# Kernel optimization log

Hardware: AMD Instinct MI355X
Metric: run time of the kernel (lower is better)

The kernel has to match this reference:

```python
import jax, jax.numpy as jnp
import numpy as np

D_WIN = 4  # local_size (max displacement); (2*D_WIN+1)^2 = 81 displacements


def avg_pool4(x):
    B, C, H, W = x.shape
    return x.reshape(B, C, H // 4, 4, W // 4, 4).mean(axis=(3, 5))


def corr_max(cur, feats, d):
    """FlowNet-style correlation (kernel=1, pad=d, max_disp=d), then max over displacements.
    cur, feats: (B,C,H,W) -> (B,H,W)."""
    B, C, H, W = cur.shape
    p = jnp.pad(feats, ((0, 0), (0, 0), (d, d), (d, d)))
    best = jnp.full((B, H, W), -jnp.inf, cur.dtype)
    for dy in range(2 * d + 1):          # small fixed 81-iteration loop
        for dx in range(2 * d + 1):
            corr = (cur * p[:, :, dy:dy + H, dx:dx + W]).sum(axis=1) / C
            best = jnp.maximum(best, corr)
    return best


def conv2d(x, w, b):
    y = jax.lax.conv_general_dilated(x, w, (1, 1), 'SAME',
                                     dimension_numbers=('NCHW', 'OIHW', 'NCHW'))
    return y + b[None, :, None, None]


def setup_inputs() -> dict:
    key = jax.random.key(0)
    ks = jax.random.split(key, 10)
    B, C, D, H, W = 8, 256, 256, 96, 96
    return {
        'cur_embed':  jax.random.normal(ks[0], (B, C, H, W), jnp.float32),
        'cur_decode': jax.random.normal(ks[1], (B, D, H, W), jnp.float32),
        'init_embed': jax.random.normal(ks[2], (B, C, H, W), jnp.float32),
        'init_seg':   jax.random.uniform(ks[3], (B, 2, H, W), jnp.float32),
        'prev_embed': jax.random.normal(ks[4], (B, C, H, W), jnp.float32),
        'prev_seg':   jax.random.uniform(ks[5], (B, 2, H, W), jnp.float32),
        'W1': jax.random.normal(ks[6], (128, 264, 3, 3), jnp.float32) * 0.02,
        'b1': jnp.zeros((128,), jnp.float32),
        'W2': jax.random.normal(ks[7], (2, 128, 3, 3), jnp.float32) * 0.02,
        'b2': jnp.zeros((2,), jnp.float32),
    }


def reference(cur_embed, cur_decode, init_embed, init_seg, prev_embed, prev_seg,
              W1, b1, W2, b2):
    B, C, H, W = cur_embed.shape
    # ---- global map: per-batch 1x1-conv similarity against pooled init feats ----
    fi = avg_pool4(init_embed)                       # (B,C,h,w)
    si = avg_pool4(init_seg)                         # (B,2,h,w)
    hw = fi.shape[2] * fi.shape[3]
    sim = jnp.einsum('bck,bchw->bkhw', fi.reshape(B, C, hw), cur_embed)  # (B,hw,H,W)
    gmap = jnp.max(sim[:, None] * si.reshape(B, 2, hw)[..., None, None], axis=2)  # (B,2,H,W)
    # ---- local map: windowed cross-correlation against masked prev feats ----
    bg = corr_max(cur_embed, prev_embed * prev_seg[:, 0:1], D_WIN)
    fg = corr_max(cur_embed, prev_embed * prev_seg[:, 1:2], D_WIN)
    lmap = jnp.stack([bg, fg], axis=1)               # (B,2,H,W)
    # ---- merge CNN ----
    h = jnp.concatenate([cur_decode, gmap, init_seg, lmap, prev_seg], axis=1)  # (B,264,H,W)
    h = jax.nn.relu(conv2d(h, W1, b1))
    out = conv2d(h, W2, b2)                          # (B,2,H,W)
    return out
```

## Files before the change

kernel.cpp:

```cpp
#include <hip/hip_runtime.h>
#include <hip/hip_bf16.h>


typedef __hip_bfloat16 bf16;
typedef __attribute__((ext_vector_type(8))) short short8;
typedef __attribute__((ext_vector_type(4))) float f32x4;

constexpr int B_  = 8;
constexpr int C_  = 256;
constexpr int H_  = 96;
constexpr int W_  = 96;
constexpr int HW_ = H_ * W_;
constexpr int PW_ = 24;
constexpr int KP_ = 576;
constexpr int KPP = 640;
constexpr int HP_ = 98;
constexpr int HPW = HP_ * HP_;
constexpr int C1O = 128;
constexpr int CHK = HPW * 32;

__device__ __forceinline__ unsigned short bfb(float f) {
    bf16 h = __float2bfloat16(f);
    return *reinterpret_cast<unsigned short*>(&h);
}

__device__ __forceinline__ void gload_lds16(const bf16* g, bf16* l) {
    __builtin_amdgcn_global_load_lds((const void*)g, (void*)l, 16, 0, 0);
}

__global__ __launch_bounds__(256)
void w1cvt_kernel(const float* __restrict__ W1, bf16* __restrict__ w1bf)
{
    int idx = blockIdx.x * 256 + threadIdx.x;
    if (idx >= 82 * 128 * 32) return;
    int ic = idx & 31;
    int oc = (idx >> 5) & 127;
    int ks = idx >> 12;
    int icc = ks / 9, tap = ks % 9;
    int icg = icc * 32 + ic;
    float v = (icg < 264) ? W1[((size_t)oc * 264 + icg) * 9 + tap] : 0.f;
    w1bf[idx] = __float2bfloat16(v);
}

__global__ __launch_bounds__(256)
void w2cvt_kernel(const float* __restrict__ W2, bf16* __restrict__ w2bf)
{
    int idx = blockIdx.x * 256 + threadIdx.x;
    if (idx >= 18 * 16 * 64) return;
    int c  = idx & 63;
    int oc = (idx >> 6) & 15;
    int s  = idx >> 10;
    int tap = s >> 1, half = s & 1;
    float v = (oc < 2) ? W2[((size_t)oc * 128 + half * 64 + c) * 9 + tap] : 0.f;
    w2bf[idx] = __float2bfloat16(v);
}

__global__ __launch_bounds__(256)
void tcur_kernel(const float* __restrict__ cur, bf16* __restrict__ curbf)
{
    __shared__ float tile[64][68];
    int b = blockIdx.z, c0 = blockIdx.y * 64, p0 = blockIdx.x * 64;
    int t = threadIdx.x;
    const float* src = cur + ((size_t)b * C_ + c0) * HW_ + p0;
    #pragma unroll
    for (int it = 0; it < 4; it++) {
        int f = t + it * 256;
        int cl = f >> 4, p4 = (f & 15) * 4;
        float4 v = *reinterpret_cast<const float4*>(src + (size_t)cl * HW_ + p4);
        *reinterpret_cast<float4*>(&tile[cl][p4]) = v;
    }
    __syncthreads();
    bf16* dst = curbf + ((size_t)b * HW_ + p0) * 256 + c0;
    #pragma unroll
    for (int it = 0; it < 4; it++) {
        int f = t + it * 256;
        int pl = f >> 4, c4 = (f & 15) * 4;
        ushort4 u;
        u.x = bfb(tile[c4 + 0][pl]); u.y = bfb(tile[c4 + 1][pl]);
        u.z = bfb(tile[c4 + 2][pl]); u.w = bfb(tile[c4 + 3][pl]);
        *reinterpret_cast<ushort4*>(dst + (size_t)pl * 256 + c4) = u;
    }
}

__global__ __launch_bounds__(256)
void pool_kernel(const float* __restrict__ init_embed,
                 const float* __restrict__ init_seg,
                 bf16* __restrict__ fibf, float* __restrict__ si)
{
    int idx = blockIdx.x * 256 + threadIdx.x;
    int total = B_ * (C_ + 2) * KPP;
    if (idx >= total) return;
    int k  = idx % KPP;
    int ch = (idx / KPP) % (C_ + 2);
    int b  = idx / (KPP * (C_ + 2));
    float s = 0.f;
    if (k < KP_) {
        int ph = k / PW_, pw = k % PW_;
        const float* src = (ch < C_)
            ? (init_embed + (((size_t)b * C_ + ch) * H_ + ph * 4) * W_ + pw * 4)
            : (init_seg   + (((size_t)b * 2 + (ch - C_)) * H_ + ph * 4) * W_ + pw * 4);
        #pragma unroll
        for (int r = 0; r < 4; r++) {
            float4 v = *reinterpret_cast<const float4*>(src + r * W_);
            s += v.x + v.y + v.z + v.w;
        }
        s *= (1.f / 16.f);
    }
    if (ch < C_) fibf[((size_t)b * KPP + k) * C_ + ch] = __float2bfloat16(s);
    else         si[(size_t)b * 2 * KPP + (ch - C_) * KPP + k] = s;
}

__global__ __launch_bounds__(256)
void gmap_mfma(const bf16* __restrict__ curbf, const bf16* __restrict__ fibf,
               const float* __restrict__ si, float* __restrict__ gout)
{
    __shared__ bf16 Abuf[8192];
    __shared__ bf16 Bbuf[8192];
    __shared__ float bred[2][2][2][64];
    int gid = blockIdx.x;
    int b = gid & 7;
    int p0 = (gid >> 3) * 128;
    int tid = threadIdx.x, lane = tid & 63;
    int w = tid >> 6, wm = w & 1, wn = w >> 1;
    int l15 = lane & 15, lk = lane >> 4;
    const bf16* fb = fibf + (size_t)b * KPP * 256;
    const bf16* cb = curbf + (size_t)b * HW_ * 256;
    const float* sib = si + (size_t)b * 2 * KPP;

    int wbase = tid & 192;
    int t3 = (tid >> 3) & 7;
    int cX = (tid & 7) ^ t3;
    int r0 = tid >> 3;
    int swzE0 = ((lk) ^ (l15 & 7)) * 8;
    int swzE1 = ((4 + lk) ^ (l15 & 7)) * 8;

    float best[2][4];
    #pragma unroll
    for (int s = 0; s < 2; s++)
        #pragma unroll
        for (int nt = 0; nt < 4; nt++) best[s][nt] = -INFINITY;
    f32x4 acc[4][4] = {};

    auto STAGE = [&](int q) {
        int chunk = q >> 2, ks = q & 3;
        int koff = ks * 64 + cX * 8;
        #pragma unroll
        for (int i = 0; i < 4; i++) {
            int row = i * 32 + r0;
            gload_lds16(fb + (size_t)(chunk * 128 + row) * 256 + koff,
                        &Abuf[(size_t)(i * 256 + wbase) * 8]);
            gload_lds16(cb + (size_t)(p0 + row) * 256 + koff,
                        &Bbuf[(size_t)(i * 256 + wbase) * 8]);
        }
    };

    auto COMPUTE = [&]() {
        #pragma unroll
        for (int k = 0; k < 2; k++) {
            int swz = k ? swzE1 : swzE0;
            short8 a[4], bq[4];
            #pragma unroll
            for (int mt = 0; mt < 4; mt++)
                a[mt] = *reinterpret_cast<const short8*>(
                    &Abuf[(size_t)(wm * 64 + mt * 16 + l15) * 64 + swz]);
            #pragma unroll
            for (int nt = 0; nt < 4; nt++)
                bq[nt] = *reinterpret_cast<const short8*>(
                    &Bbuf[(size_t)(wn * 64 + nt * 16 + l15) * 64 + swz]);
            #pragma unroll
            for (int mt = 0; mt < 4; mt++)
                #pragma unroll
                for (int nt = 0; nt < 4; nt++)
                    acc[mt][nt] = __builtin_amdgcn_mfma_f32_16x16x32_bf16(
                        a[mt], bq[nt], acc[mt][nt], 0, 0, 0);
        }
    };

    for (int q = 0; q < 20; ++q) {
        STAGE(q);
        __syncthreads();
        COMPUTE();
        if ((q & 3) == 3) {
            int kp0 = (q >> 2) * 128;
            #pragma unroll
            for (int mt = 0; mt < 4; mt++) {
                int rb = kp0 + wm * 64 + mt * 16 + lk * 4;
                float4 s0 = *reinterpret_cast<const float4*>(sib + rb);
                float4 s1 = *reinterpret_cast<const float4*>(sib + KPP + rb);
                const float* s0p = reinterpret_cast<const float*>(&s0);
                const float* s1p = reinterpret_cast<const float*>(&s1);
                #pragma unroll
                for (int nt = 0; nt < 4; nt++) {
                    #pragma unroll
                    for (int r = 0; r < 4; r++) {
                        float v = acc[mt][nt][r];
                        best[0][nt] = fmaxf(best[0][nt], v * s0p[r]);
                        best[1][nt] = fmaxf(best[1][nt], v * s1p[r]);
                    }
                    acc[mt][nt] = (f32x4){0.f, 0.f, 0.f, 0.f};
                }
            }
        }
        __syncthreads();
    }
    #pragma unroll
    for (int s = 0; s < 2; s++)
        #pragma unroll
        for (int nt = 0; nt < 4; nt++) {
            float v = best[s][nt];
            v = fmaxf(v, __shfl_xor(v, 16));
            v = fmaxf(v, __shfl_xor(v, 32));
            if (lk == 0) bred[wm][wn][s][nt * 16 + l15] = v;
        }
    __syncthreads();
    {
        int wn2 = tid >> 7, s2 = (tid >> 6) & 1, pxl = tid & 63;
        float v = fmaxf(bred[0][wn2][s2][pxl], bred[1][wn2][s2][pxl]);
        gout[((size_t)b * 2 + s2) * HW_ + p0 + wn2 * 64 + pxl] = v;
    }
}

__global__ __launch_bounds__(256)
void lmap_mfma(const bf16* __restrict__ curbf, const bf16* __restrict__ prevbf,
               const float* __restrict__ prev_seg, float* __restrict__ lout, int b0)
{
    constexpr int GSTR = 257;
    constexpr int SEGB = 64 * GSTR;
    constexpr int REDB = SEGB + 512;
    __shared__ float gl[REDB + 256];
    int b = b0 + blockIdx.y;
    const bf16* pb = prevbf + (size_t)blockIdx.y * HW_ * 256;
    const bf16* cb = curbf + (size_t)b * HW_ * 256;
    int tile = blockIdx.x;
    int ty0 = (tile / 12) * 8, tx0 = (tile % 12) * 8;
    int t = threadIdx.x, lane = t & 63, wq = t >> 6;
    int l15 = lane & 15, lk = lane >> 4;

    size_t aoff[4];
    #pragma unroll
    for (int mt = 0; mt < 4; mt++) {
        int m = mt * 16 + l15;
        int gpx = (ty0 + (m >> 3)) * W_ + tx0 + (m & 7);
        aoff[mt] = (size_t)gpx * 256 + lk * 8;
    }
    bool pred[4];
    size_t boff[4];
    int gx = tx0 - 4 + l15;
    bool colok = (gx >= 0) && (gx < W_);
    #pragma unroll
    for (int nt = 0; nt < 4; nt++) {
        int gy = ty0 - 4 + wq * 4 + nt;
        pred[nt] = colok && (gy >= 0) && (gy < H_);
        boff[nt] = pred[nt] ? ((size_t)(gy * W_ + gx) * 256 + lk * 8) : 0;
    }

    f32x4 acc[4][4] = {};
    const short8 Z8 = {0, 0, 0, 0, 0, 0, 0, 0};
    for (int kc = 0; kc < 8; kc++) {
        short8 a[4], bb[4];
        #pragma unroll
        for (int mt = 0; mt < 4; mt++)
            a[mt] = *reinterpret_cast<const short8*>(cb + aoff[mt] + kc * 32);
        #pragma unroll
        for (int nt = 0; nt < 4; nt++) {
            short8 v = Z8;
            if (pred[nt]) v = *reinterpret_cast<const short8*>(pb + boff[nt] + kc * 32);
            bb[nt] = v;
        }
        #pragma unroll
        for (int mt = 0; mt < 4; mt++)
            #pragma unroll
            for (int nt = 0; nt < 4; nt++)
                acc[mt][nt] = __builtin_amdgcn_mfma_f32_16x16x32_bf16(
                    a[mt], bb[nt], acc[mt][nt], 0, 0, 0);
    }
    #pragma unroll
    for (int mt = 0; mt < 4; mt++)
        #pragma unroll
        for (int nt = 0; nt < 4; nt++)
            #pragma unroll
            for (int r = 0; r < 4; r++)
                gl[(mt * 16 + lk * 4 + r) * GSTR + wq * 64 + nt * 16 + l15] = acc[mt][nt][r];
    #pragma unroll
    for (int it = 0; it < 2; it++) {
        int f = t + it * 256;
        int s = f >> 8, wp = f & 255;
        int wy = wp >> 4, wx = wp & 15;
        int gy = ty0 - 4 + wy, gxx = tx0 - 4 + wx;
        float v = 0.f;
        if (gy >= 0 && gy < H_ && gxx >= 0 && gxx < W_)
            v = prev_seg[((size_t)b * 2 + s) * HW_ + gy * W_ + gxx] * (1.f / 256.f);
        gl[SEGB + f] = v;
    }
    __syncthreads();
    {
        int m = t & 63;
        int sh = t >> 6;
        int s = sh >> 1, hh = sh & 1;
        int py = m >> 3, lx = m & 7;
        const float* gr = gl + m * GSTR;
        const float* sr = gl + SEGB + s * 256;
        float mx = -INFINITY;
        int wr0 = hh * 5, wr1 = hh ? 9 : 5;
        for (int wr = wr0; wr < wr1; ++wr) {
            int base = (py + wr) * 16 + lx;
            #pragma unroll
            for (int wc = 0; wc < 9; ++wc)
                mx = fmaxf(mx, gr[base + wc] * sr[base + wc]);
        }
        gl[REDB + sh * 64 + m] = mx;
    }
    __syncthreads();
    if (t < 128) {
        int s = t >> 6, m = t & 63;
        float v = fmaxf(gl[REDB + (s * 2 + 0) * 64 + m], gl[REDB + (s * 2 + 1) * 64 + m]);
        int gpx = (ty0 + (m >> 3)) * W_ + tx0 + (m & 7);
        lout[((size_t)b * 2 + s) * HW_ + gpx] = v;
    }
}

__global__ __launch_bounds__(256)
void pack_dec_kernel(const float* __restrict__ dec, bf16* __restrict__ hcat8)
{
    __shared__ float tile[64][68];
    int b = blockIdx.z, c0 = blockIdx.y * 64, p0 = blockIdx.x * 64;
    int t = threadIdx.x;
    const float* src = dec + ((size_t)b * C_ + c0) * HW_ + p0;
    #pragma unroll
    for (int it = 0; it < 4; it++) {
        int f = t + it * 256;
        int cl = f >> 4, p4 = (f & 15) * 4;
        float4 v = *reinterpret_cast<const float4*>(src + (size_t)cl * HW_ + p4);
        *reinterpret_cast<float4*>(&tile[cl][p4]) = v;
    }
    __syncthreads();
    #pragma unroll
    for (int it = 0; it < 4; it++) {
        int f = t + it * 256;
        int pl = f >> 4, c4 = (f & 15) * 4;
        int p = p0 + pl;
        int y = p / 96, x = p % 96;
        int pos = (y + 1) * HP_ + x + 1;
        int ch = c0 + c4;
        ushort4 u;
        u.x = bfb(tile[c4 + 0][pl]); u.y = bfb(tile[c4 + 1][pl]);
        u.z = bfb(tile[c4 + 2][pl]); u.w = bfb(tile[c4 + 3][pl]);
        bf16* dst = hcat8 + ((size_t)b * 8 + (ch >> 5)) * CHK + (size_t)pos * 32 + (ch & 31);
        *reinterpret_cast<ushort4*>(dst) = u;
    }
}

__global__ __launch_bounds__(256)
void pack_small_kernel(const float* __restrict__ gout,
                       const float* __restrict__ lout,
                       const float* __restrict__ init_seg,
                       const float* __restrict__ prev_seg,
                       bf16* __restrict__ hcat1)
{
    int idx = blockIdx.x * 256 + threadIdx.x;
    if (idx >= B_ * HW_) return;
    int b = idx / HW_, p = idx % HW_;
    int y = p / 96, x = p % 96;
    int pos = (y + 1) * HP_ + x + 1;
    bf16* dst = hcat1 + ((size_t)b * HPW + pos) * 8;
    float g0 = gout[((size_t)b * 2 + 0) * HW_ + p];
    float g1 = gout[((size_t)b * 2 + 1) * HW_ + p];
    float i0 = init_seg[((size_t)b * 2 + 0) * HW_ + p];
    float i1 = init_seg[((size_t)b * 2 + 1) * HW_ + p];
    float l0 = lout[((size_t)b * 2 + 0) * HW_ + p];
    float l1 = lout[((size_t)b * 2 + 1) * HW_ + p];
    float q0 = prev_seg[((size_t)b * 2 + 0) * HW_ + p];
    float q1 = prev_seg[((size_t)b * 2 + 1) * HW_ + p];
    ushort4 u; u.x = bfb(g0); u.y = bfb(g1); u.z = bfb(i0); u.w = bfb(i1);
    *reinterpret_cast<ushort4*>(dst) = u;
    ushort4 u2; u2.x = bfb(l0); u2.y = bfb(l1); u2.z = bfb(q0); u2.w = bfb(q1);
    *reinterpret_cast<ushort4*>(dst + 4) = u2;
}

__global__ __launch_bounds__(256)
void conv1_mfma(const bf16* __restrict__ hcat8, const bf16* __restrict__ hcat1,
                const bf16* __restrict__ w1bf, const float* __restrict__ b1,
                bf16* __restrict__ hmidp)
{
    __shared__ bf16 S[14336];
    bf16* Abuf = S;
    bf16* Bbuf = S + 8192;
    int gid = blockIdx.x;
    int b = gid & 7;
    int row = gid >> 3;
    int tid = threadIdx.x, lane = tid & 63;
    int w = tid >> 6, wm = w & 1, wn = w >> 1;
    int l15 = lane & 15, lk = lane >> 4;
    const bf16* hb8 = hcat8 + (size_t)b * 8 * CHK;
    const bf16* hb1 = hcat1 + (size_t)b * HPW * 8;

    int wbase = tid & 192;
    int t3 = (tid >> 3) & 7;
    int cX = (tid & 7) ^ t3;
    int selX = cX >> 2;
    int cin8 = (cX & 3) * 8;
    int r0 = tid >> 3;
    int swzE0 = ((lk) ^ (l15 & 7)) * 8;
    int swzE1 = ((4 + lk) ^ (l15 & 7)) * 8;

    f32x4 acc[4][3] = {};

    auto STAGE = [&](int p) {
        int s0 = 2 * p, s1 = s0 + 1;
        int icc0 = s0 / 9, tap0 = s0 - icc0 * 9;
        int icc1 = s1 / 9, tap1 = s1 - icc1 * 9;
        const bf16* gA = w1bf + (size_t)p * 8192 + (size_t)selX * 4096 + cin8;
        #pragma unroll
        for (int i = 0; i < 4; i++)
            gload_lds16(gA + (i * 32 + r0) * 32,
                        &Abuf[(size_t)(i * 256 + wbase) * 8]);
        int tapS = selX ? tap1 : tap0;
        int iccS = selX ? icc1 : icc0;
        int posT = (row + tapS / 3) * HP_ + (tapS % 3);
        bool is8 = (iccS >= 8);
        const bf16* gb = is8 ? hb1 : (hb8 + (size_t)iccS * CHK);
        #pragma unroll
        for (int i = 0; i < 3; i++) {
            int c = i * 32 + r0;
            const bf16* g = is8 ? (gb + (size_t)(posT + c) * 8)
                                : (gb + (size_t)(posT + c) * 32 + cin8);
            gload_lds16(g, &Bbuf[(size_t)(i * 256 + wbase) * 8]);
        }
    };

    auto COMPUTE = [&]() {
        #pragma unroll
        for (int k = 0; k < 2; k++) {
            int swz = k ? swzE1 : swzE0;
            short8 a[4], bq[3];
            #pragma unroll
            for (int mt = 0; mt < 4; mt++)
                a[mt] = *reinterpret_cast<const short8*>(
                    &Abuf[(size_t)(wm * 64 + mt * 16 + l15) * 64 + swz]);
            #pragma unroll
            for (int nt = 0; nt < 3; nt++)
                bq[nt] = *reinterpret_cast<const short8*>(
                    &Bbuf[(size_t)(wn * 48 + nt * 16 + l15) * 64 + swz]);
            #pragma unroll
            for (int mt = 0; mt < 4; mt++)
                #pragma unroll
                for (int nt = 0; nt < 3; nt++)
                    acc[mt][nt] = __builtin_amdgcn_mfma_f32_16x16x32_bf16(
                        a[mt], bq[nt], acc[mt][nt], 0, 0, 0);
        }
    };

    for (int p = 0; p < 41; ++p) {
        STAGE(p);
        __syncthreads();
        COMPUTE();
        __syncthreads();
    }

    #pragma unroll
    for (int nt = 0; nt < 3; nt++) {
        int pxl = wn * 48 + nt * 16 + l15;
        #pragma unroll
        for (int mt = 0; mt < 4; mt++) {
            int ocb = wm * 64 + mt * 16 + lk * 4;
            float4 bias = *reinterpret_cast<const float4*>(b1 + ocb);
            const float* bp = reinterpret_cast<const float*>(&bias);
            ushort4 u;
            u.x = bfb(fmaxf(acc[mt][nt][0] + bp[0], 0.f));
            u.y = bfb(fmaxf(acc[mt][nt][1] + bp[1], 0.f));
            u.z = bfb(fmaxf(acc[mt][nt][2] + bp[2], 0.f));
            u.w = bfb(fmaxf(acc[mt][nt][3] + bp[3], 0.f));
            int chunk = (ocb >> 3) ^ (pxl & 7);
            *reinterpret_cast<ushort4*>(&S[(size_t)pxl * 128 + chunk * 8 + (lk & 1) * 4]) = u;
        }
    }
    __syncthreads();
    {
        bf16* dst = hmidp + (size_t)b * HPW * 128 + ((size_t)(row + 1) * HP_ + 1) * 128;
        #pragma unroll
        for (int i = 0; i < 6; i++) {
            int f = tid + i * 256;
            int px = f >> 4, cc = f & 15;
            short8 v = *reinterpret_cast<const short8*>(
                &S[(size_t)px * 128 + (cc ^ (px & 7)) * 8]);
            *reinterpret_cast<short8*>(dst + (size_t)f * 8) = v;
        }
    }
}

__global__ __launch_bounds__(256)
void conv2_mfma(const bf16* __restrict__ hmidp, const bf16* __restrict__ w2bf,
                const float* __restrict__ b2, float* __restrict__ out)
{
    __shared__ bf16 Abuf[1024];
    __shared__ bf16 Bbuf[8192];
    int gid = blockIdx.x;
    int b = gid & 7;
    int p0 = (gid >> 3) * 128;
    int tid = threadIdx.x, lane = tid & 63;
    int wn = tid >> 6;
    int l15 = lane & 15, lk = lane >> 4;
    const bf16* hb = hmidp + (size_t)b * HPW * 128;

    int wbase = tid & 192;
    int t3 = (tid >> 3) & 7;
    int cX = (tid & 7) ^ t3;
    int r0 = tid >> 3;
    int posB[4];
    #pragma unroll
    for (int i = 0; i < 4; i++) {
        int px = p0 + i * 32 + r0;
        posB[i] = (px / 96) * HP_ + (px % 96);
    }
    int swzE0 = ((lk) ^ (l15 & 7)) * 8;
    int swzE1 = ((4 + lk) ^ (l15 & 7)) * 8;

    f32x4 acc[2] = {};

    auto STAGE = [&](int s) {
        int tap = s >> 1, half = s & 1;
        int toff = (tap / 3) * HP_ + (tap % 3);
        if (tid < 128)
            gload_lds16(w2bf + ((size_t)s * 16 + r0) * 64 + cX * 8,
                        &Abuf[(size_t)(tid & 192) * 8]);
        #pragma unroll
        for (int i = 0; i < 4; i++)
            gload_lds16(hb + (size_t)(posB[i] + toff) * 128 + half * 64 + cX * 8,
                        &Bbuf[(size_t)(i * 256 + wbase) * 8]);
    };

    auto COMPUTE = [&]() {
        #pragma unroll
        for (int k = 0; k < 2; k++) {
            int swz = k ? swzE1 : swzE0;
            short8 a = *reinterpret_cast<const short8*>(&Abuf[(size_t)l15 * 64 + swz]);
            #pragma unroll
            for (int nt = 0; nt < 2; nt++) {
                short8 bq = *reinterpret_cast<const short8*>(
                    &Bbuf[(size_t)(wn * 32 + nt * 16 + l15) * 64 + swz]);
                acc[nt] = __builtin_amdgcn_mfma_f32_16x16x32_bf16(a, bq, acc[nt], 0, 0, 0);
            }
        }
    };

    for (int s = 0; s < 18; ++s) {
        STAGE(s);
        __syncthreads();
        COMPUTE();
        __syncthreads();
    }

    if (lk == 0) {
        float bb0 = b2[0], bb1 = b2[1];
        #pragma unroll
        for (int nt = 0; nt < 2; nt++) {
            int px = p0 + wn * 32 + nt * 16 + l15;
            out[((size_t)b * 2 + 0) * HW_ + px] = acc[nt][0] + bb0;
            out[((size_t)b * 2 + 1) * HW_ + px] = acc[nt][1] + bb1;
        }
    }
}

extern "C" void kernel_launch(void* const* d_in, const int* in_sizes, int n_in,
                              void* d_out, int out_size, void* d_ws, size_t ws_size,
                              hipStream_t stream)
{
    const float* cur_embed  = (const float*)d_in[0];
    const float* cur_decode = (const float*)d_in[1];
    const float* init_embed = (const float*)d_in[2];
    const float* init_seg   = (const float*)d_in[3];
    const float* prev_embed = (const float*)d_in[4];
    const float* prev_seg   = (const float*)d_in[5];
    const float* W1 = (const float*)d_in[6];
    const float* b1 = (const float*)d_in[7];
    const float* W2 = (const float*)d_in[8];
    const float* b2 = (const float*)d_in[9];
    float* out = (float*)d_out;

    char* ws = (char*)d_ws;
    bf16* hcat8 = (bf16*)ws;
    bf16* curbf = (bf16*)ws;
    bf16* hcat1 = (bf16*)(ws + 39337984);
    const size_t HCAT_REGION = 40567296;
    const size_t HMID_SIZE   = 19668992;
    bf16* hmidp  = (bf16*)(ws + HCAT_REGION);
    bf16* fibf   = (bf16*)(ws + HCAT_REGION);
    bf16* prevbf = (bf16*)(ws + HCAT_REGION);
    float* si  = (float*)(ws + HCAT_REGION + 2621440);
    bf16* w1bf = (bf16*)(ws + 60236288);
    bf16* w2bf = (bf16*)(ws + 60908032);
    float* gout = (float*)(ws + 60944896);
    float* lout = (float*)(ws + 61534720);

    { int total = 82 * 128 * 32;
      w1cvt_kernel<<<(total + 255) / 256, 256, 0, stream>>>(W1, w1bf); }
    { int total = 18 * 16 * 64;
      w2cvt_kernel<<<(total + 255) / 256, 256, 0, stream>>>(W2, w2bf); }
    { dim3 g(144, 4, B_);
      tcur_kernel<<<g, 256, 0, stream>>>(cur_embed, curbf); }
    { int total = B_ * (C_ + 2) * KPP;
      pool_kernel<<<(total + 255) / 256, 256, 0, stream>>>(init_embed, init_seg, fibf, si); }
    { gmap_mfma<<<576, 256, 0, stream>>>(curbf, fibf, si, gout); }
    for (int g = 0; g < 2; g++) {
        dim3 gt(144, 4, 4);
        tcur_kernel<<<gt, 256, 0, stream>>>(prev_embed + (size_t)g * 4 * C_ * HW_, prevbf);
        dim3 gl(144, 4);
        lmap_mfma<<<gl, 256, 0, stream>>>(curbf, prevbf, prev_seg, lout, g * 4);
    }
    hipMemsetAsync(ws, 0, HCAT_REGION + HMID_SIZE, stream);
    { dim3 g(144, 4, B_);
      pack_dec_kernel<<<g, 256, 0, stream>>>(cur_decode, hcat8); }
    { int total = B_ * HW_;
      pack_small_kernel<<<(total + 255) / 256, 256, 0, stream>>>(gout, lout, init_seg, prev_seg, hcat1); }
    { conv1_mfma<<<768, 256, 0, stream>>>(hcat8, hcat1, w1bf, b1, hmidp); }
    { conv2_mfma<<<576, 256, 0, stream>>>(hmidp, w2bf, b2, out); }
}
```

Baseline: 287.7 us.

## Stage lmap operands through swizzled LDS and zero only padded borders

The local-correlation kernel now stages A and B tiles into swizzled shared memory with direct global-to-LDS loads, reading out-of-range window rows from a zero buffer instead of using predicated register loads. The full-workspace memset before packing is replaced by a small kernel that zeroes only the one-pixel padding border of the concatenated input and hidden buffers. This cuts tens of megabytes of memset traffic and gives more coalesced operand loads. It relies on the interior being fully overwritten and on the zero buffer sitting in a region of the weight buffer that stays zero.

```diff
diff --git a/kernel.cpp b/kernel.cpp
--- a/kernel.cpp
+++ b/kernel.cpp
@@ -222,68 +222,86 @@
 
 __global__ __launch_bounds__(256)
 void lmap_mfma(const bf16* __restrict__ curbf, const bf16* __restrict__ prevbf,
+               const bf16* __restrict__ zbuf,
                const float* __restrict__ prev_seg, float* __restrict__ lout, int b0)
 {
     constexpr int GSTR = 257;
     constexpr int SEGB = 64 * GSTR;
     constexpr int REDB = SEGB + 512;
-    __shared__ float gl[REDB + 256];
+    __shared__ __align__(16) char Smem[(REDB + 256) * 4];
+    bf16* Abuf = (bf16*)Smem;
+    bf16* Bbuf = (bf16*)(Smem + 8192);
+    float* gl  = (float*)Smem;
+
     int b = b0 + blockIdx.y;
     const bf16* pb = prevbf + (size_t)blockIdx.y * HW_ * 256;
     const bf16* cb = curbf + (size_t)b * HW_ * 256;
     int tile = blockIdx.x;
     int ty0 = (tile / 12) * 8, tx0 = (tile % 12) * 8;
-    int t = threadIdx.x, lane = t & 63, wq = t >> 6;
+    int tid = threadIdx.x, lane = tid & 63, wn = tid >> 6;
     int l15 = lane & 15, lk = lane >> 4;
 
-    size_t aoff[4];
-    #pragma unroll
-    for (int mt = 0; mt < 4; mt++) {
-        int m = mt * 16 + l15;
-        int gpx = (ty0 + (m >> 3)) * W_ + tx0 + (m & 7);
-        aoff[mt] = (size_t)gpx * 256 + lk * 8;
-    }
-    bool pred[4];
-    size_t boff[4];
-    int gx = tx0 - 4 + l15;
-    bool colok = (gx >= 0) && (gx < W_);
-    #pragma unroll
-    for (int nt = 0; nt < 4; nt++) {
-        int gy = ty0 - 4 + wq * 4 + nt;
-        pred[nt] = colok && (gy >= 0) && (gy < H_);
-        boff[nt] = pred[nt] ? ((size_t)(gy * W_ + gx) * 256 + lk * 8) : 0;
+    int wbase = tid & 192;
+    int t3 = (tid >> 3) & 7;
+    int cX = (tid & 7) ^ t3;
+    int r0 = tid >> 3;
+    int swzE0 = ((lk) ^ (l15 & 7)) * 8;
+    int swzE1 = ((4 + lk) ^ (l15 & 7)) * 8;
+
+    int gpxA0 = (ty0 + (r0 >> 3)) * W_ + tx0 + (r0 & 7);
+    int gpxA1 = (ty0 + (r0 >> 3) + 4) * W_ + tx0 + (r0 & 7);
+    const bf16* rowB[8];
+    #pragma unroll
+    for (int i = 0; i < 8; i++) {
+        int wrow = i * 32 + r0;
+        int wy = wrow >> 4, wx = wrow & 15;
+        int gy = ty0 - 4 + wy, gx = tx0 - 4 + wx;
+        bool ok = (gy >= 0) && (gy < H_) && (gx >= 0) && (gx < W_);
+        rowB[i] = ok ? (pb + (size_t)(gy * W_ + gx) * 256) : zbuf;
     }
 
     f32x4 acc[4][4] = {};
-    const short8 Z8 = {0, 0, 0, 0, 0, 0, 0, 0};
-    for (int kc = 0; kc < 8; kc++) {
-        short8 a[4], bb[4];
-        #pragma unroll
-        for (int mt = 0; mt < 4; mt++)
-            a[mt] = *reinterpret_cast<const short8*>(cb + aoff[mt] + kc * 32);
-        #pragma unroll
-        for (int nt = 0; nt < 4; nt++) {
-            short8 v = Z8;
-            if (pred[nt]) v = *reinterpret_cast<const short8*>(pb + boff[nt] + kc * 32);
-            bb[nt] = v;
-        }
-        #pragma unroll
-        for (int mt = 0; mt < 4; mt++)
+
+    for (int ks = 0; ks < 4; ++ks) {
+        int koff = ks * 64 + cX * 8;
+        gload_lds16(cb + (size_t)gpxA0 * 256 + koff, &Abuf[(size_t)(wbase) * 8]);
+        gload_lds16(cb + (size_t)gpxA1 * 256 + koff, &Abuf[(size_t)(256 + wbase) * 8]);
+        #pragma unroll
+        for (int i = 0; i < 8; i++)
+            gload_lds16(rowB[i] + koff, &Bbuf[(size_t)(i * 256 + wbase) * 8]);
+        __syncthreads();
+        #pragma unroll
+        for (int k = 0; k < 2; k++) {
+            int swz = k ? swzE1 : swzE0;
+            short8 a[4], bq[4];
+            #pragma unroll
+            for (int mt = 0; mt < 4; mt++)
+                a[mt] = *reinterpret_cast<const short8*>(
+                    &Abuf[(size_t)(mt * 16 + l15) * 64 + swz]);
             #pragma unroll
             for (int nt = 0; nt < 4; nt++)
-                acc[mt][nt] = __builtin_amdgcn_mfma_f32_16x16x32_bf16(
-                    a[mt], bb[nt], acc[mt][nt], 0, 0, 0);
-    }
+                bq[nt] = *reinterpret_cast<const short8*>(
+                    &Bbuf[(size_t)(wn * 64 + nt * 16 + l15) * 64 + swz]);
+            #pragma unroll
+            for (int mt = 0; mt < 4; mt++)
+                #pragma unroll
+                for (int nt = 0; nt < 4; nt++)
+                    acc[mt][nt] = __builtin_amdgcn_mfma_f32_16x16x32_bf16(
+                        a[mt], bq[nt], acc[mt][nt], 0, 0, 0);
+        }
+        __syncthreads();
+    }
+
     #pragma unroll
     for (int mt = 0; mt < 4; mt++)
         #pragma unroll
         for (int nt = 0; nt < 4; nt++)
             #pragma unroll
             for (int r = 0; r < 4; r++)
-                gl[(mt * 16 + lk * 4 + r) * GSTR + wq * 64 + nt * 16 + l15] = acc[mt][nt][r];
+                gl[(mt * 16 + lk * 4 + r) * GSTR + wn * 64 + nt * 16 + l15] = acc[mt][nt][r];
     #pragma unroll
     for (int it = 0; it < 2; it++) {
-        int f = t + it * 256;
+        int f = tid + it * 256;
         int s = f >> 8, wp = f & 255;
         int wy = wp >> 4, wx = wp & 15;
         int gy = ty0 - 4 + wy, gxx = tx0 - 4 + wx;
@@ -294,8 +312,8 @@
     }
     __syncthreads();
     {
-        int m = t & 63;
-        int sh = t >> 6;
+        int m = tid & 63;
+        int sh = tid >> 6;
         int s = sh >> 1, hh = sh & 1;
         int py = m >> 3, lx = m & 7;
         const float* gr = gl + m * GSTR;
@@ -311,8 +329,8 @@
         gl[REDB + sh * 64 + m] = mx;
     }
     __syncthreads();
-    if (t < 128) {
-        int s = t >> 6, m = t & 63;
+    if (tid < 128) {
+        int s = tid >> 6, m = tid & 63;
         float v = fmaxf(gl[REDB + (s * 2 + 0) * 64 + m], gl[REDB + (s * 2 + 1) * 64 + m]);
         int gpx = (ty0 + (m >> 3)) * W_ + tx0 + (m & 7);
         lout[((size_t)b * 2 + s) * HW_ + gpx] = v;
@@ -378,6 +396,33 @@
 }
 
 __global__ __launch_bounds__(256)
+void zero_border_kernel(bf16* __restrict__ hcat8, bf16* __restrict__ hcat1,
+                        bf16* __restrict__ hmidp)
+{
+    int idx = blockIdx.x * 256 + threadIdx.x;
+    if (idx >= B_ * 388) return;
+    int b = idx / 388, bi = idx % 388;
+    int pos;
+    if (bi < 98) pos = bi;
+    else if (bi < 196) pos = 97 * HP_ + (bi - 98);
+    else if (bi < 292) pos = (bi - 196 + 1) * HP_;
+    else pos = (bi - 292 + 1) * HP_ + 97;
+    const short8 Z = {0, 0, 0, 0, 0, 0, 0, 0};
+    #pragma unroll
+    for (int c = 0; c < 8; c++) {
+        bf16* p = hcat8 + ((size_t)b * 8 + c) * CHK + (size_t)pos * 32;
+        #pragma unroll
+        for (int j = 0; j < 4; j++)
+            *reinterpret_cast<short8*>(p + j * 8) = Z;
+    }
+    *reinterpret_cast<short8*>(hcat1 + ((size_t)b * HPW + pos) * 8) = Z;
+    bf16* q = hmidp + ((size_t)b * HPW + pos) * 128;
+    #pragma unroll
+    for (int j = 0; j < 16; j++)
+        *reinterpret_cast<short8*>(q + j * 8) = Z;
+}
+
+__global__ __launch_bounds__(256)
 void conv1_mfma(const bf16* __restrict__ hcat8, const bf16* __restrict__ hcat1,
                 const bf16* __restrict__ w1bf, const float* __restrict__ b1,
                 bf16* __restrict__ hmidp)
@@ -582,7 +627,6 @@
     bf16* curbf = (bf16*)ws;
     bf16* hcat1 = (bf16*)(ws + 39337984);
     const size_t HCAT_REGION = 40567296;
-    const size_t HMID_SIZE   = 19668992;
     bf16* hmidp  = (bf16*)(ws + HCAT_REGION);
     bf16* fibf   = (bf16*)(ws + HCAT_REGION);
     bf16* prevbf = (bf16*)(ws + HCAT_REGION);
@@ -591,6 +635,7 @@
     bf16* w2bf = (bf16*)(ws + 60908032);
     float* gout = (float*)(ws + 60944896);
     float* lout = (float*)(ws + 61534720);
+    const bf16* zbuf = w1bf + (size_t)81 * 4096;
 
     { int total = 82 * 128 * 32;
       w1cvt_kernel<<<(total + 255) / 256, 256, 0, stream>>>(W1, w1bf); }
@@ -605,9 +650,10 @@
         dim3 gt(144, 4, 4);
         tcur_kernel<<<gt, 256, 0, stream>>>(prev_embed + (size_t)g * 4 * C_ * HW_, prevbf);
         dim3 gl(144, 4);
-        lmap_mfma<<<gl, 256, 0, stream>>>(curbf, prevbf, prev_seg, lout, g * 4);
-    }
-    hipMemsetAsync(ws, 0, HCAT_REGION + HMID_SIZE, stream);
+        lmap_mfma<<<gl, 256, 0, stream>>>(curbf, prevbf, zbuf, prev_seg, lout, g * 4);
+    }
+    { int total = B_ * 388;
+      zero_border_kernel<<<(total + 255) / 256, 256, 0, stream>>>(hcat8, hcat1, hmidp); }
     { dim3 g(144, 4, B_);
       pack_dec_kernel<<<g, 256, 0, stream>>>(cur_decode, hcat8); }
     { int total = B_ * HW_;
```

After: 264.1 us. 8.2% less time.
